# Kernel tuning notes

Measured on AMD Instinct MI355X. Metric: run time of the kernel, lower is better.

Reference implementation:

```python
import jax, jax.numpy as jnp
import numpy as np
from jax import lax

C = 320
GN_GROUPS = 32
EPS = 1e-5


def setup_inputs() -> dict:
    key = jax.random.key(0)
    ks = jax.random.split(key, 5)
    x = jax.random.normal(ks[0], (16, C, 96, 96), dtype=jnp.float32)
    # depthwise 3x3 kernel [C,1,3,3] (OIHW with feature_group_count=C)
    dw_w = jax.random.normal(ks[1], (C, 1, 3, 3), dtype=jnp.float32) * 0.1
    dw_b = jax.random.normal(ks[2], (C,), dtype=jnp.float32) * 0.01
    gn_w = jnp.ones((C,), dtype=jnp.float32)
    gn_b = jnp.zeros((C,), dtype=jnp.float32)
    proj_w = jax.random.normal(ks[3], (C,), dtype=jnp.float32) * 0.001
    proj_b = jnp.full((1,), -4.0, dtype=jnp.float32)
    return {"x": x, "dw_w": dw_w, "dw_b": dw_b, "gn_w": gn_w,
            "gn_b": gn_b, "proj_w": proj_w, "proj_b": proj_b}


def _group_norm(h, gamma, beta):
    # h: [B,C,H,W]; GN over (C//G, H, W) within each of G groups; biased var (torch)
    B, Cc, H, W = h.shape
    hg = h.reshape(B, GN_GROUPS, Cc // GN_GROUPS, H, W)
    mean = jnp.mean(hg, axis=(2, 3, 4), keepdims=True)
    var = jnp.mean(jnp.square(hg - mean), axis=(2, 3, 4), keepdims=True)
    hn = ((hg - mean) * lax.rsqrt(var + EPS)).reshape(B, Cc, H, W)
    return hn * gamma[None, :, None, None] + beta[None, :, None, None]


def reference(x, dw_w, dw_b, gn_w, gn_b, proj_w, proj_b):
    # depthwise 3x3 conv, padding=1
    h = lax.conv_general_dilated(
        x, dw_w, window_strides=(1, 1), padding=((1, 1), (1, 1)),
        dimension_numbers=("NCHW", "OIHW", "NCHW"), feature_group_count=C)
    h = h + dw_b[None, :, None, None]
    h = _group_norm(h, gn_w, gn_b)
    # 1x1 conv C -> 1 == per-pixel channel dot product
    g = jnp.einsum("bchw,c->bhw", h, proj_w) + proj_b[0]
    return jax.nn.sigmoid(g)[:, None, :, :]  # [B,1,H,W]
```

## Files before the change

### kernel.cpp

```cpp
#include <hip/hip_runtime.h>
#include <math.h>

#define HH 96
#define WW 96
#define NPIX (HH*WW)
#define CC 320
#define GG 32
#define CPG 10
#define YT 3
#define TPB 512

__global__ __launch_bounds__(TPB)
void k_main(const float* __restrict__ x, const float* __restrict__ dw_w,
            const float* __restrict__ dw_b, const float* __restrict__ gn_w,
            const float* __restrict__ proj_w,
            float* __restrict__ P, float* __restrict__ partials) {
  const int bid = blockIdx.x;
  const int yt = bid % YT;
  const int t  = bid / YT;
  const int gr = t & 31;
  const int b  = t >> 5;

  __shared__ float wsm[CPG * 9], ssm[CPG], bsm[CPG];
  const int tid = threadIdx.x;
  if (tid < CPG * 9) wsm[tid] = dw_w[gr * CPG * 9 + tid];
  if (tid < CPG) {
    int c = gr * CPG + tid;
    ssm[tid] = proj_w[c] * gn_w[c];
    bsm[tid] = dw_b[c];
  }
  __syncthreads();

  const int lane = tid & 63;
  const int xcl  = tid & 31;
  const int r    = tid >> 5;
  const bool active = xcl < 24;
  const float mact  = active ? 1.f : 0.f;
  const int xc = min(xcl, 23);
  const int Y0 = yt * 32 + 2 * r;
  const int Y1 = Y0 + 1;

  const float ma = (Y0 > 0)      ? 1.f : 0.f;
  const float md = (Y1 < HH - 1) ? 1.f : 0.f;
  const int ya = max(Y0 - 1, 0);
  const int yd = min(Y1 + 1, HH - 1);
  const float mlft = (xcl > 0)  ? 1.f : 0.f;
  const float mrgt = (xcl < 23) ? 1.f : 0.f;
  const int lm1 = (xcl >= 1) ? lane - 1 : lane;
  const int lp1 = (xcl < 31) ? lane + 1 : lane;

  const size_t offa = (size_t)ya * WW + xc * 4;
  const size_t offb = (size_t)Y0 * WW + xc * 4;
  const size_t offc = (size_t)Y1 * WW + xc * 4;
  const size_t offd = (size_t)yd * WW + xc * 4;
  const float* xg = x + ((size_t)(b * CC + gr * CPG)) * NPIX;

  float p0=0.f,p1=0.f,p2=0.f,p3=0.f,p4=0.f,p5=0.f,p6=0.f,p7=0.f;
  float s1 = 0.f, s2 = 0.f;

  float4 A = *(const float4*)(xg + offa);
  float4 B = *(const float4*)(xg + offb);
  float4 C = *(const float4*)(xg + offc);
  float4 D = *(const float4*)(xg + offd);

  #pragma unroll 1
  for (int ch = 0; ch < CPG; ++ch) {
    const float* nimg = xg + (size_t)min(ch + 1, CPG - 1) * NPIX;
    float4 nA = *(const float4*)(nimg + offa);
    float4 nB = *(const float4*)(nimg + offb);
    float4 nC = *(const float4*)(nimg + offc);
    float4 nD = *(const float4*)(nimg + offd);

    A.x *= ma; A.y *= ma; A.z *= ma; A.w *= ma;
    D.x *= md; D.y *= md; D.z *= md; D.w *= md;

    float al = __shfl(A.w, lm1) * mlft;
    float bl = __shfl(B.w, lm1) * mlft;
    float cl2 = __shfl(C.w, lm1) * mlft;
    float dl = __shfl(D.w, lm1) * mlft;
    float ar = __shfl(A.x, lp1) * mrgt;
    float br = __shfl(B.x, lp1) * mrgt;
    float cr = __shfl(C.x, lp1) * mrgt;
    float dr = __shfl(D.x, lp1) * mrgt;

    const float* wp = &wsm[ch * 9];
    const float w0 = wp[0], w1 = wp[1], w2 = wp[2];
    const float w3 = wp[3], w4 = wp[4], w5 = wp[5];
    const float w6 = wp[6], w7 = wp[7], w8 = wp[8];

    float u0 = w0*al  + w1*A.x + w2*A.y + w3*bl  + w4*B.x + w5*B.y + w6*cl2 + w7*C.x + w8*C.y;
    float u1 = w0*A.x + w1*A.y + w2*A.z + w3*B.x + w4*B.y + w5*B.z + w6*C.x + w7*C.y + w8*C.z;
    float u2 = w0*A.y + w1*A.z + w2*A.w + w3*B.y + w4*B.z + w5*B.w + w6*C.y + w7*C.z + w8*C.w;
    float u3 = w0*A.z + w1*A.w + w2*ar  + w3*B.z + w4*B.w + w5*br  + w6*C.z + w7*C.w + w8*cr;
    float u4 = w0*bl  + w1*B.x + w2*B.y + w3*cl2 + w4*C.x + w5*C.y + w6*dl  + w7*D.x + w8*D.y;
    float u5 = w0*B.x + w1*B.y + w2*B.z + w3*C.x + w4*C.y + w5*C.z + w6*D.x + w7*D.y + w8*D.z;
    float u6 = w0*B.y + w1*B.z + w2*B.w + w3*C.y + w4*C.z + w5*C.w + w6*D.y + w7*D.z + w8*D.w;
    float u7 = w0*B.z + w1*B.w + w2*br  + w3*C.z + w4*C.w + w5*cr  + w6*D.z + w7*D.w + w8*dr;

    const float sc = ssm[ch], bias = bsm[ch];
    p0 = fmaf(sc, u0, p0); p1 = fmaf(sc, u1, p1);
    p2 = fmaf(sc, u2, p2); p3 = fmaf(sc, u3, p3);
    p4 = fmaf(sc, u4, p4); p5 = fmaf(sc, u5, p5);
    p6 = fmaf(sc, u6, p6); p7 = fmaf(sc, u7, p7);

    float h0 = u0 + bias, h1 = u1 + bias, h2 = u2 + bias, h3 = u3 + bias;
    float h4 = u4 + bias, h5 = u5 + bias, h6 = u6 + bias, h7 = u7 + bias;
    s1 += mact * (((h0 + h1) + (h2 + h3)) + ((h4 + h5) + (h6 + h7)));
    float q0 = fmaf(h0, h0, h1 * h1), q1 = fmaf(h2, h2, h3 * h3);
    float q2 = fmaf(h4, h4, h5 * h5), q3 = fmaf(h6, h6, h7 * h7);
    s2 += mact * ((q0 + q1) + (q2 + q3));

    A = nA; B = nB; C = nC; D = nD;
  }

  if (active) {
    size_t base = ((size_t)(b * GG + gr)) * NPIX + (size_t)Y0 * WW + xcl * 4;
    *(float4*)&P[base]      = make_float4(p0, p1, p2, p3);
    *(float4*)&P[base + WW] = make_float4(p4, p5, p6, p7);
  }

  #pragma unroll
  for (int off = 32; off; off >>= 1) {
    s1 += __shfl_down(s1, off);
    s2 += __shfl_down(s2, off);
  }
  __shared__ float r1[8], r2[8];
  if ((tid & 63) == 0) { r1[tid >> 6] = s1; r2[tid >> 6] = s2; }
  __syncthreads();
  if (tid == 0) {
    float a = 0.f, q = 0.f;
    #pragma unroll
    for (int i = 0; i < 8; ++i) { a += r1[i]; q += r2[i]; }
    size_t o = (((size_t)(b * GG + gr)) * YT + yt) * 2;
    partials[o]     = a;
    partials[o + 1] = q;
  }
}

__global__ __launch_bounds__(256)
void k_out(const float* __restrict__ P, const float* __restrict__ partials,
           const float* __restrict__ dw_b, const float* __restrict__ gn_w,
           const float* __restrict__ gn_b, const float* __restrict__ proj_w,
           const float* __restrict__ proj_b, float* __restrict__ out) {
  const int b   = blockIdx.x / 9;
  const int blk = blockIdx.x % 9;
  __shared__ float rs[GG];
  __shared__ float Ds;

  if (threadIdx.x < GG) {
    const int gr = threadIdx.x;
    float s1 = 0.f, s2 = 0.f;
    #pragma unroll
    for (int t = 0; t < YT; ++t) {
      size_t o = (((size_t)(b * GG + gr)) * YT + t) * 2;
      s1 += partials[o];
      s2 += partials[o + 1];
    }
    const float invN = 1.f / (float)(CPG * NPIX);
    float mean = s1 * invN;
    float var  = s2 * invN - mean * mean;
    float rinv = rsqrtf(var + 1e-5f);
    rs[gr] = rinv;
    float K = 0.f, E = 0.f;
    #pragma unroll
    for (int i = 0; i < CPG; ++i) {
      int c = gr * CPG + i;
      float pg = proj_w[c] * gn_w[c];
      K = fmaf(pg, dw_b[c] - mean, K);
      E = fmaf(proj_w[c], gn_b[c], E);
    }
    float contrib = fmaf(rinv, K, E);
    #pragma unroll
    for (int m = 16; m; m >>= 1) contrib += __shfl_xor(contrib, m, 32);
    if (gr == 0) Ds = contrib + proj_b[0];
  }
  __syncthreads();

  const int p = (blk * 256 + threadIdx.x) * 4;
  const float* Pb = P + (size_t)b * GG * NPIX + p;
  float g0 = 0.f, g1 = 0.f, g2 = 0.f, g3 = 0.f;
  #pragma unroll 8
  for (int gr = 0; gr < GG; ++gr) {
    float4 v = *(const float4*)(Pb + (size_t)gr * NPIX);
    float rr = rs[gr];
    g0 = fmaf(rr, v.x, g0);
    g1 = fmaf(rr, v.y, g1);
    g2 = fmaf(rr, v.z, g2);
    g3 = fmaf(rr, v.w, g3);
  }
  const float d = Ds;
  float4 o;
  o.x = 1.f / (1.f + expf(-(g0 + d)));
  o.y = 1.f / (1.f + expf(-(g1 + d)));
  o.z = 1.f / (1.f + expf(-(g2 + d)));
  o.w = 1.f / (1.f + expf(-(g3 + d)));
  *(float4*)&out[(size_t)b * NPIX + p] = o;
}

extern "C" void kernel_launch(void* const* d_in, const int* in_sizes, int n_in,
                              void* d_out, int out_size, void* d_ws, size_t ws_size,
                              hipStream_t stream) {
  const float* x      = (const float*)d_in[0];
  const float* dw_w   = (const float*)d_in[1];
  const float* dw_b   = (const float*)d_in[2];
  const float* gn_w   = (const float*)d_in[3];
  const float* gn_b   = (const float*)d_in[4];
  const float* proj_w = (const float*)d_in[5];
  const float* proj_b = (const float*)d_in[6];
  float* out = (float*)d_out;

  const size_t P_BYTES = (size_t)16 * GG * NPIX * 4;
  float* P        = (float*)d_ws;
  float* partials = (float*)((char*)d_ws + P_BYTES);

  hipLaunchKernelGGL(k_main, dim3(16 * GG * YT), dim3(TPB), 0, stream,
                     x, dw_w, dw_b, gn_w, proj_w, P, partials);
  hipLaunchKernelGGL(k_out, dim3(16 * 9), dim3(256), 0, stream,
                     P, partials, dw_b, gn_w, gn_b, proj_w, proj_b, out);
}
```

Before: 52.25 us.

## Store intermediate projection in fp16, merge row tiles into one block per group

The intermediate per-group projection buffer P now holds fp16 instead of fp32, which halves the write traffic in the main kernel and the read traffic in the output kernel. Each main-kernel block now covers all three row tiles of a (batch, group) pair, so the grid shrinks from 1536 to 512 blocks and the partial-sum reduction across tiles goes away. The per-channel prefetch double-buffering is removed in favour of an unrolled loop that issues twelve loads per channel. The output kernel uses more, smaller blocks. Risks are fp16 precision loss in P and lower occupancy or weaker latency hiding from the larger per-thread register footprint and fewer blocks.

```diff
diff --git a/kernel.cpp b/kernel.cpp
--- a/kernel.cpp
+++ b/kernel.cpp
@@ -7,19 +7,17 @@
 #define CC 320
 #define GG 32
 #define CPG 10
-#define YT 3
 #define TPB 512
+
+typedef _Float16 half4v __attribute__((ext_vector_type(4)));
 
 __global__ __launch_bounds__(TPB)
 void k_main(const float* __restrict__ x, const float* __restrict__ dw_w,
             const float* __restrict__ dw_b, const float* __restrict__ gn_w,
             const float* __restrict__ proj_w,
-            float* __restrict__ P, float* __restrict__ partials) {
-  const int bid = blockIdx.x;
-  const int yt = bid % YT;
-  const int t  = bid / YT;
-  const int gr = t & 31;
-  const int b  = t >> 5;
+            _Float16* __restrict__ P, float* __restrict__ partials) {
+  const int gr = blockIdx.x & 31;
+  const int b  = blockIdx.x >> 5;
 
   __shared__ float wsm[CPG * 9], ssm[CPG], bsm[CPG];
   const int tid = threadIdx.x;
@@ -37,86 +35,101 @@
   const bool active = xcl < 24;
   const float mact  = active ? 1.f : 0.f;
   const int xc = min(xcl, 23);
-  const int Y0 = yt * 32 + 2 * r;
-  const int Y1 = Y0 + 1;
-
-  const float ma = (Y0 > 0)      ? 1.f : 0.f;
-  const float md = (Y1 < HH - 1) ? 1.f : 0.f;
-  const int ya = max(Y0 - 1, 0);
-  const int yd = min(Y1 + 1, HH - 1);
   const float mlft = (xcl > 0)  ? 1.f : 0.f;
   const float mrgt = (xcl < 23) ? 1.f : 0.f;
   const int lm1 = (xcl >= 1) ? lane - 1 : lane;
   const int lp1 = (xcl < 31) ? lane + 1 : lane;
 
-  const size_t offa = (size_t)ya * WW + xc * 4;
-  const size_t offb = (size_t)Y0 * WW + xc * 4;
-  const size_t offc = (size_t)Y1 * WW + xc * 4;
-  const size_t offd = (size_t)yd * WW + xc * 4;
+  int   offa[3], offb[3], offc[3], offd[3];
+  float ma[3], md[3];
+  #pragma unroll
+  for (int g3 = 0; g3 < 3; ++g3) {
+    const int Y0 = 2 * r + 32 * g3;
+    const int Y1 = Y0 + 1;
+    ma[g3] = (Y0 > 0)      ? 1.f : 0.f;
+    md[g3] = (Y1 < HH - 1) ? 1.f : 0.f;
+    const int ya = max(Y0 - 1, 0);
+    const int yd = min(Y1 + 1, HH - 1);
+    offa[g3] = ya * WW + xc * 4;
+    offb[g3] = Y0 * WW + xc * 4;
+    offc[g3] = Y1 * WW + xc * 4;
+    offd[g3] = yd * WW + xc * 4;
+  }
   const float* xg = x + ((size_t)(b * CC + gr * CPG)) * NPIX;
 
-  float p0=0.f,p1=0.f,p2=0.f,p3=0.f,p4=0.f,p5=0.f,p6=0.f,p7=0.f;
+  float p[24];
+  #pragma unroll
+  for (int i = 0; i < 24; ++i) p[i] = 0.f;
   float s1 = 0.f, s2 = 0.f;
-
-  float4 A = *(const float4*)(xg + offa);
-  float4 B = *(const float4*)(xg + offb);
-  float4 C = *(const float4*)(xg + offc);
-  float4 D = *(const float4*)(xg + offd);
 
   #pragma unroll 1
   for (int ch = 0; ch < CPG; ++ch) {
-    const float* nimg = xg + (size_t)min(ch + 1, CPG - 1) * NPIX;
-    float4 nA = *(const float4*)(nimg + offa);
-    float4 nB = *(const float4*)(nimg + offb);
-    float4 nC = *(const float4*)(nimg + offc);
-    float4 nD = *(const float4*)(nimg + offd);
-
-    A.x *= ma; A.y *= ma; A.z *= ma; A.w *= ma;
-    D.x *= md; D.y *= md; D.z *= md; D.w *= md;
-
-    float al = __shfl(A.w, lm1) * mlft;
-    float bl = __shfl(B.w, lm1) * mlft;
-    float cl2 = __shfl(C.w, lm1) * mlft;
-    float dl = __shfl(D.w, lm1) * mlft;
-    float ar = __shfl(A.x, lp1) * mrgt;
-    float br = __shfl(B.x, lp1) * mrgt;
-    float cr = __shfl(C.x, lp1) * mrgt;
-    float dr = __shfl(D.x, lp1) * mrgt;
-
+    const float* img = xg + ch * NPIX;
     const float* wp = &wsm[ch * 9];
     const float w0 = wp[0], w1 = wp[1], w2 = wp[2];
     const float w3 = wp[3], w4 = wp[4], w5 = wp[5];
     const float w6 = wp[6], w7 = wp[7], w8 = wp[8];
-
-    float u0 = w0*al  + w1*A.x + w2*A.y + w3*bl  + w4*B.x + w5*B.y + w6*cl2 + w7*C.x + w8*C.y;
-    float u1 = w0*A.x + w1*A.y + w2*A.z + w3*B.x + w4*B.y + w5*B.z + w6*C.x + w7*C.y + w8*C.z;
-    float u2 = w0*A.y + w1*A.z + w2*A.w + w3*B.y + w4*B.z + w5*B.w + w6*C.y + w7*C.z + w8*C.w;
-    float u3 = w0*A.z + w1*A.w + w2*ar  + w3*B.z + w4*B.w + w5*br  + w6*C.z + w7*C.w + w8*cr;
-    float u4 = w0*bl  + w1*B.x + w2*B.y + w3*cl2 + w4*C.x + w5*C.y + w6*dl  + w7*D.x + w8*D.y;
-    float u5 = w0*B.x + w1*B.y + w2*B.z + w3*C.x + w4*C.y + w5*C.z + w6*D.x + w7*D.y + w8*D.z;
-    float u6 = w0*B.y + w1*B.z + w2*B.w + w3*C.y + w4*C.z + w5*C.w + w6*D.y + w7*D.z + w8*D.w;
-    float u7 = w0*B.z + w1*B.w + w2*br  + w3*C.z + w4*C.w + w5*cr  + w6*D.z + w7*D.w + w8*dr;
-
     const float sc = ssm[ch], bias = bsm[ch];
-    p0 = fmaf(sc, u0, p0); p1 = fmaf(sc, u1, p1);
-    p2 = fmaf(sc, u2, p2); p3 = fmaf(sc, u3, p3);
-    p4 = fmaf(sc, u4, p4); p5 = fmaf(sc, u5, p5);
-    p6 = fmaf(sc, u6, p6); p7 = fmaf(sc, u7, p7);
-
-    float h0 = u0 + bias, h1 = u1 + bias, h2 = u2 + bias, h3 = u3 + bias;
-    float h4 = u4 + bias, h5 = u5 + bias, h6 = u6 + bias, h7 = u7 + bias;
-    s1 += mact * (((h0 + h1) + (h2 + h3)) + ((h4 + h5) + (h6 + h7)));
-    float q0 = fmaf(h0, h0, h1 * h1), q1 = fmaf(h2, h2, h3 * h3);
-    float q2 = fmaf(h4, h4, h5 * h5), q3 = fmaf(h6, h6, h7 * h7);
-    s2 += mact * ((q0 + q1) + (q2 + q3));
-
-    A = nA; B = nB; C = nC; D = nD;
+
+    #pragma unroll
+    for (int g3 = 0; g3 < 3; ++g3) {
+      float4 A = *(const float4*)(img + offa[g3]);
+      float4 B = *(const float4*)(img + offb[g3]);
+      float4 C = *(const float4*)(img + offc[g3]);
+      float4 D = *(const float4*)(img + offd[g3]);
+      const float mma = ma[g3], mmd = md[g3];
+      A.x *= mma; A.y *= mma; A.z *= mma; A.w *= mma;
+      D.x *= mmd; D.y *= mmd; D.z *= mmd; D.w *= mmd;
+
+      float al = __shfl(A.w, lm1) * mlft;
+      float bl = __shfl(B.w, lm1) * mlft;
+      float cl2 = __shfl(C.w, lm1) * mlft;
+      float dl = __shfl(D.w, lm1) * mlft;
+      float ar = __shfl(A.x, lp1) * mrgt;
+      float br = __shfl(B.x, lp1) * mrgt;
+      float cr = __shfl(C.x, lp1) * mrgt;
+      float dr = __shfl(D.x, lp1) * mrgt;
+
+      float u0 = w0*al  + w1*A.x + w2*A.y + w3*bl  + w4*B.x + w5*B.y + w6*cl2 + w7*C.x + w8*C.y;
+      float u1 = w0*A.x + w1*A.y + w2*A.z + w3*B.x + w4*B.y + w5*B.z + w6*C.x + w7*C.y + w8*C.z;
+      float u2 = w0*A.y + w1*A.z + w2*A.w + w3*B.y + w4*B.z + w5*B.w + w6*C.y + w7*C.z + w8*C.w;
+      float u3 = w0*A.z + w1*A.w + w2*ar  + w3*B.z + w4*B.w + w5*br  + w6*C.z + w7*C.w + w8*cr;
+      float u4 = w0*bl  + w1*B.x + w2*B.y + w3*cl2 + w4*C.x + w5*C.y + w6*dl  + w7*D.x + w8*D.y;
+      float u5 = w0*B.x + w1*B.y + w2*B.z + w3*C.x + w4*C.y + w5*C.z + w6*D.x + w7*D.y + w8*D.z;
+      float u6 = w0*B.y + w1*B.z + w2*B.w + w3*C.y + w4*C.z + w5*C.w + w6*D.y + w7*D.z + w8*D.w;
+      float u7 = w0*B.z + w1*B.w + w2*br  + w3*C.z + w4*C.w + w5*cr  + w6*D.z + w7*D.w + w8*dr;
+
+      p[g3*8+0] = fmaf(sc, u0, p[g3*8+0]);
+      p[g3*8+1] = fmaf(sc, u1, p[g3*8+1]);
+      p[g3*8+2] = fmaf(sc, u2, p[g3*8+2]);
+      p[g3*8+3] = fmaf(sc, u3, p[g3*8+3]);
+      p[g3*8+4] = fmaf(sc, u4, p[g3*8+4]);
+      p[g3*8+5] = fmaf(sc, u5, p[g3*8+5]);
+      p[g3*8+6] = fmaf(sc, u6, p[g3*8+6]);
+      p[g3*8+7] = fmaf(sc, u7, p[g3*8+7]);
+
+      float h0 = u0 + bias, h1 = u1 + bias, h2 = u2 + bias, h3 = u3 + bias;
+      float h4 = u4 + bias, h5 = u5 + bias, h6 = u6 + bias, h7 = u7 + bias;
+      s1 += mact * (((h0 + h1) + (h2 + h3)) + ((h4 + h5) + (h6 + h7)));
+      float q0 = fmaf(h0, h0, h1 * h1), q1 = fmaf(h2, h2, h3 * h3);
+      float q2 = fmaf(h4, h4, h5 * h5), q3 = fmaf(h6, h6, h7 * h7);
+      s2 += mact * ((q0 + q1) + (q2 + q3));
+    }
   }
 
   if (active) {
-    size_t base = ((size_t)(b * GG + gr)) * NPIX + (size_t)Y0 * WW + xcl * 4;
-    *(float4*)&P[base]      = make_float4(p0, p1, p2, p3);
-    *(float4*)&P[base + WW] = make_float4(p4, p5, p6, p7);
+    _Float16* Pp = P + ((size_t)(b * GG + gr)) * NPIX;
+    #pragma unroll
+    for (int g3 = 0; g3 < 3; ++g3) {
+      const int Y0 = 2 * r + 32 * g3;
+      half4v h0, h1;
+      h0.x = (_Float16)p[g3*8+0]; h0.y = (_Float16)p[g3*8+1];
+      h0.z = (_Float16)p[g3*8+2]; h0.w = (_Float16)p[g3*8+3];
+      h1.x = (_Float16)p[g3*8+4]; h1.y = (_Float16)p[g3*8+5];
+      h1.z = (_Float16)p[g3*8+6]; h1.w = (_Float16)p[g3*8+7];
+      *(half4v*)&Pp[(size_t)Y0 * WW + xcl * 4]       = h0;
+      *(half4v*)&Pp[(size_t)(Y0 + 1) * WW + xcl * 4] = h1;
+    }
   }
 
   #pragma unroll
@@ -131,31 +144,25 @@
     float a = 0.f, q = 0.f;
     #pragma unroll
     for (int i = 0; i < 8; ++i) { a += r1[i]; q += r2[i]; }
-    size_t o = (((size_t)(b * GG + gr)) * YT + yt) * 2;
-    partials[o]     = a;
-    partials[o + 1] = q;
+    partials[blockIdx.x * 2]     = a;
+    partials[blockIdx.x * 2 + 1] = q;
   }
 }
 
-__global__ __launch_bounds__(256)
-void k_out(const float* __restrict__ P, const float* __restrict__ partials,
+__global__ __launch_bounds__(128)
+void k_out(const _Float16* __restrict__ P, const float* __restrict__ partials,
            const float* __restrict__ dw_b, const float* __restrict__ gn_w,
            const float* __restrict__ gn_b, const float* __restrict__ proj_w,
            const float* __restrict__ proj_b, float* __restrict__ out) {
-  const int b   = blockIdx.x / 9;
-  const int blk = blockIdx.x % 9;
+  const int b   = blockIdx.x / 18;
+  const int blk = blockIdx.x % 18;
   __shared__ float rs[GG];
   __shared__ float Ds;
 
   if (threadIdx.x < GG) {
     const int gr = threadIdx.x;
-    float s1 = 0.f, s2 = 0.f;
-    #pragma unroll
-    for (int t = 0; t < YT; ++t) {
-      size_t o = (((size_t)(b * GG + gr)) * YT + t) * 2;
-      s1 += partials[o];
-      s2 += partials[o + 1];
-    }
+    float s1 = partials[(b * GG + gr) * 2];
+    float s2 = partials[(b * GG + gr) * 2 + 1];
     const float invN = 1.f / (float)(CPG * NPIX);
     float mean = s1 * invN;
     float var  = s2 * invN - mean * mean;
@@ -176,17 +183,17 @@
   }
   __syncthreads();
 
-  const int p = (blk * 256 + threadIdx.x) * 4;
-  const float* Pb = P + (size_t)b * GG * NPIX + p;
+  const int p = (blk * 128 + threadIdx.x) * 4;
+  const _Float16* Pb = P + (size_t)b * GG * NPIX + p;
   float g0 = 0.f, g1 = 0.f, g2 = 0.f, g3 = 0.f;
-  #pragma unroll 8
+  #pragma unroll
   for (int gr = 0; gr < GG; ++gr) {
-    float4 v = *(const float4*)(Pb + (size_t)gr * NPIX);
+    half4v v = *(const half4v*)(Pb + (size_t)gr * NPIX);
     float rr = rs[gr];
-    g0 = fmaf(rr, v.x, g0);
-    g1 = fmaf(rr, v.y, g1);
-    g2 = fmaf(rr, v.z, g2);
-    g3 = fmaf(rr, v.w, g3);
+    g0 = fmaf(rr, (float)v.x, g0);
+    g1 = fmaf(rr, (float)v.y, g1);
+    g2 = fmaf(rr, (float)v.z, g2);
+    g3 = fmaf(rr, (float)v.w, g3);
   }
   const float d = Ds;
   float4 o;
@@ -209,12 +216,12 @@
   const float* proj_b = (const float*)d_in[6];
   float* out = (float*)d_out;
 
-  const size_t P_BYTES = (size_t)16 * GG * NPIX * 4;
-  float* P        = (float*)d_ws;
+  const size_t P_BYTES = (size_t)16 * GG * NPIX * 2;
+  _Float16* P     = (_Float16*)d_ws;
   float* partials = (float*)((char*)d_ws + P_BYTES);
 
-  hipLaunchKernelGGL(k_main, dim3(16 * GG * YT), dim3(TPB), 0, stream,
+  hipLaunchKernelGGL(k_main, dim3(16 * GG), dim3(TPB), 0, stream,
                      x, dw_w, dw_b, gn_w, proj_w, P, partials);
-  hipLaunchKernelGGL(k_out, dim3(16 * 9), dim3(256), 0, stream,
+  hipLaunchKernelGGL(k_out, dim3(16 * 18), dim3(128), 0, stream,
                      P, partials, dw_b, gn_w, gn_b, proj_w, proj_b, out);
 }
```

Measured after the change: 51.76 us. No clear change (-0.9%).

## Retile depthwise conv to 3-column lanes with smaller blocks and no prefetch

Applied to the files above, without the earlier changes.

Each thread in the main kernel now covers 3 columns by 2 rows, loaded as float3, so all 32 lanes of a half-wave are active instead of 24 of 32. Blocks shrink to 256 threads with twice as many row tiles, and launch bounds ask for 8 blocks per CU. The register double-buffered prefetch of the next channel is removed, leaving latency hiding to higher occupancy. The output kernel uses twice as many 128-thread blocks with a fully unrolled group loop. The risk is that float3 accesses are unaligned to 16 bytes and may split into narrower, less efficient memory instructions.

```diff
diff --git a/kernel.cpp b/kernel.cpp
--- a/kernel.cpp
+++ b/kernel.cpp
@@ -7,10 +7,10 @@
 #define CC 320
 #define GG 32
 #define CPG 10
-#define YT 3
-#define TPB 512
-
-__global__ __launch_bounds__(TPB)
+#define YT 6
+#define TPB 256
+
+__global__ __launch_bounds__(TPB, 8)
 void k_main(const float* __restrict__ x, const float* __restrict__ dw_w,
             const float* __restrict__ dw_b, const float* __restrict__ gn_w,
             const float* __restrict__ proj_w,
@@ -34,89 +34,78 @@
   const int lane = tid & 63;
   const int xcl  = tid & 31;
   const int r    = tid >> 5;
-  const bool active = xcl < 24;
-  const float mact  = active ? 1.f : 0.f;
-  const int xc = min(xcl, 23);
-  const int Y0 = yt * 32 + 2 * r;
+  const int col0 = 3 * xcl;
+  const int Y0 = yt * 16 + 2 * r;
   const int Y1 = Y0 + 1;
 
-  const float ma = (Y0 > 0)      ? 1.f : 0.f;
-  const float md = (Y1 < HH - 1) ? 1.f : 0.f;
+  const float mtop = (Y0 > 0)      ? 1.f : 0.f;
+  const float mbot = (Y1 < HH - 1) ? 1.f : 0.f;
   const int ya = max(Y0 - 1, 0);
   const int yd = min(Y1 + 1, HH - 1);
   const float mlft = (xcl > 0)  ? 1.f : 0.f;
-  const float mrgt = (xcl < 23) ? 1.f : 0.f;
+  const float mrgt = (xcl < 31) ? 1.f : 0.f;
   const int lm1 = (xcl >= 1) ? lane - 1 : lane;
   const int lp1 = (xcl < 31) ? lane + 1 : lane;
 
-  const size_t offa = (size_t)ya * WW + xc * 4;
-  const size_t offb = (size_t)Y0 * WW + xc * 4;
-  const size_t offc = (size_t)Y1 * WW + xc * 4;
-  const size_t offd = (size_t)yd * WW + xc * 4;
+  const int offa = ya * WW + col0;
+  const int offb = Y0 * WW + col0;
+  const int offc = Y1 * WW + col0;
+  const int offd = yd * WW + col0;
   const float* xg = x + ((size_t)(b * CC + gr * CPG)) * NPIX;
 
-  float p0=0.f,p1=0.f,p2=0.f,p3=0.f,p4=0.f,p5=0.f,p6=0.f,p7=0.f;
+  float p0=0.f,p1=0.f,p2=0.f,p3=0.f,p4=0.f,p5=0.f;
   float s1 = 0.f, s2 = 0.f;
-
-  float4 A = *(const float4*)(xg + offa);
-  float4 B = *(const float4*)(xg + offb);
-  float4 C = *(const float4*)(xg + offc);
-  float4 D = *(const float4*)(xg + offd);
 
   #pragma unroll 1
   for (int ch = 0; ch < CPG; ++ch) {
-    const float* nimg = xg + (size_t)min(ch + 1, CPG - 1) * NPIX;
-    float4 nA = *(const float4*)(nimg + offa);
-    float4 nB = *(const float4*)(nimg + offb);
-    float4 nC = *(const float4*)(nimg + offc);
-    float4 nD = *(const float4*)(nimg + offd);
-
-    A.x *= ma; A.y *= ma; A.z *= ma; A.w *= ma;
-    D.x *= md; D.y *= md; D.z *= md; D.w *= md;
-
-    float al = __shfl(A.w, lm1) * mlft;
-    float bl = __shfl(B.w, lm1) * mlft;
-    float cl2 = __shfl(C.w, lm1) * mlft;
-    float dl = __shfl(D.w, lm1) * mlft;
-    float ar = __shfl(A.x, lp1) * mrgt;
-    float br = __shfl(B.x, lp1) * mrgt;
-    float cr = __shfl(C.x, lp1) * mrgt;
-    float dr = __shfl(D.x, lp1) * mrgt;
+    const float* img = xg + ch * NPIX;
+    float3 A = *(const float3*)(img + offa);
+    float3 B = *(const float3*)(img + offb);
+    float3 C = *(const float3*)(img + offc);
+    float3 D = *(const float3*)(img + offd);
+    A.x *= mtop; A.y *= mtop; A.z *= mtop;
+    D.x *= mbot; D.y *= mbot; D.z *= mbot;
+
+    float La = __shfl(A.z, lm1) * mlft;
+    float Lb = __shfl(B.z, lm1) * mlft;
+    float Lc = __shfl(C.z, lm1) * mlft;
+    float Ld = __shfl(D.z, lm1) * mlft;
+    float Ta = __shfl(A.x, lp1) * mrgt;
+    float Tb = __shfl(B.x, lp1) * mrgt;
+    float Tc = __shfl(C.x, lp1) * mrgt;
+    float Td = __shfl(D.x, lp1) * mrgt;
 
     const float* wp = &wsm[ch * 9];
     const float w0 = wp[0], w1 = wp[1], w2 = wp[2];
     const float w3 = wp[3], w4 = wp[4], w5 = wp[5];
     const float w6 = wp[6], w7 = wp[7], w8 = wp[8];
-
-    float u0 = w0*al  + w1*A.x + w2*A.y + w3*bl  + w4*B.x + w5*B.y + w6*cl2 + w7*C.x + w8*C.y;
+    const float sc = ssm[ch], bias = bsm[ch];
+
+    float u0 = w0*La  + w1*A.x + w2*A.y + w3*Lb  + w4*B.x + w5*B.y + w6*Lc  + w7*C.x + w8*C.y;
     float u1 = w0*A.x + w1*A.y + w2*A.z + w3*B.x + w4*B.y + w5*B.z + w6*C.x + w7*C.y + w8*C.z;
-    float u2 = w0*A.y + w1*A.z + w2*A.w + w3*B.y + w4*B.z + w5*B.w + w6*C.y + w7*C.z + w8*C.w;
-    float u3 = w0*A.z + w1*A.w + w2*ar  + w3*B.z + w4*B.w + w5*br  + w6*C.z + w7*C.w + w8*cr;
-    float u4 = w0*bl  + w1*B.x + w2*B.y + w3*cl2 + w4*C.x + w5*C.y + w6*dl  + w7*D.x + w8*D.y;
-    float u5 = w0*B.x + w1*B.y + w2*B.z + w3*C.x + w4*C.y + w5*C.z + w6*D.x + w7*D.y + w8*D.z;
-    float u6 = w0*B.y + w1*B.z + w2*B.w + w3*C.y + w4*C.z + w5*C.w + w6*D.y + w7*D.z + w8*D.w;
-    float u7 = w0*B.z + w1*B.w + w2*br  + w3*C.z + w4*C.w + w5*cr  + w6*D.z + w7*D.w + w8*dr;
-
-    const float sc = ssm[ch], bias = bsm[ch];
-    p0 = fmaf(sc, u0, p0); p1 = fmaf(sc, u1, p1);
-    p2 = fmaf(sc, u2, p2); p3 = fmaf(sc, u3, p3);
-    p4 = fmaf(sc, u4, p4); p5 = fmaf(sc, u5, p5);
-    p6 = fmaf(sc, u6, p6); p7 = fmaf(sc, u7, p7);
-
-    float h0 = u0 + bias, h1 = u1 + bias, h2 = u2 + bias, h3 = u3 + bias;
-    float h4 = u4 + bias, h5 = u5 + bias, h6 = u6 + bias, h7 = u7 + bias;
-    s1 += mact * (((h0 + h1) + (h2 + h3)) + ((h4 + h5) + (h6 + h7)));
-    float q0 = fmaf(h0, h0, h1 * h1), q1 = fmaf(h2, h2, h3 * h3);
-    float q2 = fmaf(h4, h4, h5 * h5), q3 = fmaf(h6, h6, h7 * h7);
-    s2 += mact * ((q0 + q1) + (q2 + q3));
-
-    A = nA; B = nB; C = nC; D = nD;
-  }
-
-  if (active) {
-    size_t base = ((size_t)(b * GG + gr)) * NPIX + (size_t)Y0 * WW + xcl * 4;
-    *(float4*)&P[base]      = make_float4(p0, p1, p2, p3);
-    *(float4*)&P[base + WW] = make_float4(p4, p5, p6, p7);
+    float u2 = w0*A.y + w1*A.z + w2*Ta  + w3*B.y + w4*B.z + w5*Tb  + w6*C.y + w7*C.z + w8*Tc;
+    float u3 = w0*Lb  + w1*B.x + w2*B.y + w3*Lc  + w4*C.x + w5*C.y + w6*Ld  + w7*D.x + w8*D.y;
+    float u4 = w0*B.x + w1*B.y + w2*B.z + w3*C.x + w4*C.y + w5*C.z + w6*D.x + w7*D.y + w8*D.z;
+    float u5 = w0*B.y + w1*B.z + w2*Tb  + w3*C.y + w4*C.z + w5*Tc  + w6*D.y + w7*D.z + w8*Td;
+
+    p0 = fmaf(sc, u0, p0); p1 = fmaf(sc, u1, p1); p2 = fmaf(sc, u2, p2);
+    p3 = fmaf(sc, u3, p3); p4 = fmaf(sc, u4, p4); p5 = fmaf(sc, u5, p5);
+
+    float h0 = u0 + bias, h1 = u1 + bias, h2 = u2 + bias;
+    float h3 = u3 + bias, h4 = u4 + bias, h5 = u5 + bias;
+    s1 += ((h0 + h1) + (h2 + h3)) + (h4 + h5);
+    float q0 = fmaf(h0, h0, h1 * h1);
+    float q1 = fmaf(h2, h2, h3 * h3);
+    float q2 = fmaf(h4, h4, h5 * h5);
+    s2 += (q0 + q1) + q2;
+  }
+
+  {
+    float* Pp = P + ((size_t)(b * GG + gr)) * NPIX;
+    float3 v0; v0.x = p0; v0.y = p1; v0.z = p2;
+    float3 v1; v1.x = p3; v1.y = p4; v1.z = p5;
+    *(float3*)&Pp[offb] = v0;
+    *(float3*)&Pp[offc] = v1;
   }
 
   #pragma unroll
@@ -124,26 +113,24 @@
     s1 += __shfl_down(s1, off);
     s2 += __shfl_down(s2, off);
   }
-  __shared__ float r1[8], r2[8];
+  __shared__ float r1[4], r2[4];
   if ((tid & 63) == 0) { r1[tid >> 6] = s1; r2[tid >> 6] = s2; }
   __syncthreads();
   if (tid == 0) {
-    float a = 0.f, q = 0.f;
-    #pragma unroll
-    for (int i = 0; i < 8; ++i) { a += r1[i]; q += r2[i]; }
-    size_t o = (((size_t)(b * GG + gr)) * YT + yt) * 2;
-    partials[o]     = a;
-    partials[o + 1] = q;
+    float a = r1[0] + r1[1] + r1[2] + r1[3];
+    float q = r2[0] + r2[1] + r2[2] + r2[3];
+    partials[bid * 2]     = a;
+    partials[bid * 2 + 1] = q;
   }
 }
 
-__global__ __launch_bounds__(256)
+__global__ __launch_bounds__(128)
 void k_out(const float* __restrict__ P, const float* __restrict__ partials,
            const float* __restrict__ dw_b, const float* __restrict__ gn_w,
            const float* __restrict__ gn_b, const float* __restrict__ proj_w,
            const float* __restrict__ proj_b, float* __restrict__ out) {
-  const int b   = blockIdx.x / 9;
-  const int blk = blockIdx.x % 9;
+  const int b   = blockIdx.x / 18;
+  const int blk = blockIdx.x % 18;
   __shared__ float rs[GG];
   __shared__ float Ds;
 
@@ -152,7 +139,7 @@
     float s1 = 0.f, s2 = 0.f;
     #pragma unroll
     for (int t = 0; t < YT; ++t) {
-      size_t o = (((size_t)(b * GG + gr)) * YT + t) * 2;
+      int o = (((b * GG + gr) * YT) + t) * 2;
       s1 += partials[o];
       s2 += partials[o + 1];
     }
@@ -176,10 +163,10 @@
   }
   __syncthreads();
 
-  const int p = (blk * 256 + threadIdx.x) * 4;
+  const int p = (blk * 128 + threadIdx.x) * 4;
   const float* Pb = P + (size_t)b * GG * NPIX + p;
   float g0 = 0.f, g1 = 0.f, g2 = 0.f, g3 = 0.f;
-  #pragma unroll 8
+  #pragma unroll
   for (int gr = 0; gr < GG; ++gr) {
     float4 v = *(const float4*)(Pb + (size_t)gr * NPIX);
     float rr = rs[gr];
@@ -215,6 +202,6 @@
 
   hipLaunchKernelGGL(k_main, dim3(16 * GG * YT), dim3(TPB), 0, stream,
                      x, dw_w, dw_b, gn_w, proj_w, P, partials);
-  hipLaunchKernelGGL(k_out, dim3(16 * 9), dim3(256), 0, stream,
+  hipLaunchKernelGGL(k_out, dim3(16 * 18), dim3(128), 0, stream,
                      P, partials, dw_b, gn_w, gn_b, proj_w, proj_b, out);
 }
```

Result: faster. 46.88 us, median of 4 (-10.3%).
